# Kernel optimization log

Measured on AMD Instinct MI355X. Metric: run time of the kernel, lower is better.

Reference implementation:

```python
import jax, jax.numpy as jnp
import numpy as np

# dims
B_, L_, DIN, H, DOUT, NL = 2, 1024, 512, 768, 512, 4
ED, N, K = H, 16, 4            # expand_factor=1 -> d_inner=H; d_state=16; d_conv=4
DTR = (H + 15) // 16           # dt_rank = ceil(d_model/16) = 48


def setup_inputs() -> dict:
    key = jax.random.key(0)
    ks = iter(jax.random.split(key, 32))
    def g(shape, s=0.02):
        return jax.random.normal(next(ks), shape, jnp.float32) * s
    inp = dict(
        x=jax.random.normal(next(ks), (B_, L_, DIN), jnp.float32),
        in_proj_w=g((H, DIN)), in_proj_b=jnp.zeros((H,), jnp.float32),
        out_proj_w=g((DOUT, H)), out_proj_b=jnp.zeros((DOUT,), jnp.float32),
        ln1_w=jnp.ones((NL, H), jnp.float32), ln1_b=jnp.zeros((NL, H), jnp.float32),
        ln2_w=jnp.ones((NL, H), jnp.float32), ln2_b=jnp.zeros((NL, H), jnp.float32),
        ffn_w1=g((NL, 4 * H, H)), ffn_b1=jnp.zeros((NL, 4 * H), jnp.float32),
        ffn_w2=g((NL, H, 4 * H)), ffn_b2=jnp.zeros((NL, H), jnp.float32),
        rms_w=jnp.ones((NL, ED), jnp.float32),
        m_in_w=g((NL, 2 * ED, H)),
        conv_w=g((NL, ED, 1, K), 0.2), conv_b=jnp.zeros((NL, ED), jnp.float32),
        xproj_w=g((NL, DTR + 2 * N, ED)),
        dt_w=g((NL, ED, DTR), 0.1), dt_b=g((NL, ED), 0.1),
        A_log=jnp.log(jnp.tile(jnp.arange(1, N + 1, dtype=jnp.float32), (NL, ED, 1))),
        Dp=jnp.ones((NL, ED), jnp.float32),
        m_out_w=g((NL, H, ED)),
    )
    return inp


def _layernorm(x, w, b):
    m = x.mean(-1, keepdims=True)
    v = ((x - m) ** 2).mean(-1, keepdims=True)
    return (x - m) / jnp.sqrt(v + 1e-5) * w + b


def _rmsnorm(x, w):
    return x * jax.lax.rsqrt((x * x).mean(-1, keepdims=True) + 1e-5) * w


def _selective_scan(dA, dBx):
    # h_t = dA_t * h_{t-1} + dBx_t, done as a parallel associative scan over L
    def comb(c1, c2):
        a1, b1 = c1
        a2, b2 = c2
        return a1 * a2, a2 * b1 + b2
    _, h = jax.lax.associative_scan(comb, (dA, dBx), axis=1)
    return h  # (B, L, ED, N)


def _mamba(x, rw, iw, cw, cb, xw, dw, db, Alog, Dp, ow):
    # mambapy ResidualBlock: x + MambaBlock(RMSNorm(x))
    xn = _rmsnorm(x, rw)
    xz = xn @ iw.T                             # (B, L, 2*ED)
    xi, z = jnp.split(xz, 2, axis=-1)
    # causal depthwise conv1d (padding = K-1 left)
    xc = jax.lax.conv_general_dilated(
        xi.transpose(0, 2, 1), cw, (1,), [(K - 1, 0)],
        feature_group_count=ED, dimension_numbers=('NCH', 'OIH', 'NCH'))
    xi = jax.nn.silu(xc.transpose(0, 2, 1) + cb)
    dbc = xi @ xw.T                            # (B, L, DTR + 2N)
    d = dbc[..., :DTR]
    Bm = dbc[..., DTR:DTR + N]
    Cm = dbc[..., DTR + N:]
    delta = jax.nn.softplus(d @ dw.T + db)     # (B, L, ED)
    A = -jnp.exp(Alog)                         # (ED, N)
    dA = jnp.exp(delta[..., None] * A)         # (B, L, ED, N)
    dBx = (delta * xi)[..., None] * Bm[:, :, None, :]
    h = _selective_scan(dA, dBx)
    y = jnp.einsum('blen,bln->ble', h, Cm) + Dp * xi
    y = y * jax.nn.silu(z)
    return x + y @ ow.T


def reference(x, in_proj_w, in_proj_b, out_proj_w, out_proj_b,
              ln1_w, ln1_b, ln2_w, ln2_b,
              ffn_w1, ffn_b1, ffn_w2, ffn_b2,
              rms_w, m_in_w, conv_w, conv_b, xproj_w,
              dt_w, dt_b, A_log, Dp, m_out_w):
    h = x @ in_proj_w.T + in_proj_b
    for i in range(NL):
        h = h + _mamba(_layernorm(h, ln1_w[i], ln1_b[i]),
                       rms_w[i], m_in_w[i], conv_w[i], conv_b[i], xproj_w[i],
                       dt_w[i], dt_b[i], A_log[i], Dp[i], m_out_w[i])
        hn = _layernorm(h, ln2_w[i], ln2_b[i])
        h = h + jax.nn.relu(hn @ ffn_w1[i].T + ffn_b1[i]) @ ffn_w2[i].T + ffn_b2[i]
    return h @ out_proj_w.T + out_proj_b
```

## Files before the change

### kernel.cpp

```cpp
#include <hip/hip_runtime.h>
#include <stdint.h>

typedef unsigned short u16;
typedef __attribute__((ext_vector_type(8))) short short8;
typedef __attribute__((ext_vector_type(4))) float f32x4;

static __device__ __forceinline__ u16 f2bf(float f){
  unsigned int x = __float_as_uint(f);
  unsigned int r = (x + 0x7FFFu + ((x >> 16) & 1u)) >> 16;
  return (u16)r;
}
static __device__ __forceinline__ float bf2f(u16 u){
  return __uint_as_float(((unsigned int)u) << 16);
}

__global__ __launch_bounds__(256) void prep_cvt(
    const float* __restrict__ s0, const float* __restrict__ s1,
    const float* __restrict__ s2, const float* __restrict__ s3,
    const float* __restrict__ s4, const float* __restrict__ s5,
    const float* __restrict__ s6,
    u16* __restrict__ d0, u16* __restrict__ d1, u16* __restrict__ d2,
    u16* __restrict__ d3, u16* __restrict__ d4, u16* __restrict__ d5,
    u16* __restrict__ d6){
  size_t i = ((size_t)blockIdx.x * 256 + threadIdx.x) * 8;
  const float* src; u16* dst; size_t base;
  if      (i <  1048576){ src = s0; dst = d0; base = 0; }
  else if (i <  1441792){ src = s1; dst = d1; base = 1048576; }
  else if (i <  1835008){ src = s2; dst = d2; base = 1441792; }
  else if (i <  6553600){ src = s3; dst = d3; base = 1835008; }
  else if (i <  8912896){ src = s4; dst = d4; base = 6553600; }
  else if (i < 18350080){ src = s5; dst = d5; base = 8912896; }
  else                  { src = s6; dst = d6; base = 18350080; }
  size_t o = i - base;
  #pragma unroll
  for (int p = 0; p < 2; p++){
    float4 v = *reinterpret_cast<const float4*>(src + o + p * 4);
    union { u16 u[4]; unsigned long long ll; } t;
    t.u[0] = f2bf(v.x); t.u[1] = f2bf(v.y); t.u[2] = f2bf(v.z); t.u[3] = f2bf(v.w);
    *reinterpret_cast<unsigned long long*>(dst + o + p * 4) = t.ll;
  }
}

__global__ __launch_bounds__(256) void build_dbc(const float* __restrict__ dt_w,
                                                 const float* __restrict__ xproj_w,
                                                 u16* __restrict__ out){
  const int total = 4 * 896 * 768;
  for (int idx = blockIdx.x * 256 + threadIdx.x; idx < total; idx += gridDim.x * 256){
    int l = idx / (896 * 768);
    int rem = idx - l * 896 * 768;
    int row = rem / 768;
    int k = rem - row * 768;
    float v = 0.f;
    if (row < 768){
      const float* dtr = dt_w + ((size_t)l * 768 + row) * 48;
      const float* xp  = xproj_w + (size_t)l * 80 * 768 + k;
      #pragma unroll 8
      for (int j = 0; j < 48; j++) v += dtr[j] * xp[(size_t)j * 768];
    } else if (row < 800){
      v = xproj_w[(size_t)l * 80 * 768 + (size_t)(48 + row - 768) * 768 + k];
    }
    out[idx] = f2bf(v);
  }
}

__global__ __launch_bounds__(256) void ln_rms_kernel(const float* __restrict__ in,
                                                     const float* __restrict__ w,
                                                     const float* __restrict__ b,
                                                     const float* __restrict__ rw,
                                                     float* __restrict__ xln,
                                                     u16* __restrict__ outB){
  int row = blockIdx.x;
  const float* x = in + (size_t)row * 768;
  int t = threadIdx.x;
  float v0 = x[t], v1 = x[t + 256], v2 = x[t + 512];
  float s = v0 + v1 + v2;
  float s2 = v0 * v0 + v1 * v1 + v2 * v2;
  #pragma unroll
  for (int off = 1; off < 64; off <<= 1){ s += __shfl_xor(s, off); s2 += __shfl_xor(s2, off); }
  __shared__ float red[8];
  int wid = t >> 6, lane = t & 63;
  if (lane == 0){ red[wid] = s; red[4 + wid] = s2; }
  __syncthreads();
  s = red[0] + red[1] + red[2] + red[3];
  s2 = red[4] + red[5] + red[6] + red[7];
  float mean = s * (1.f / 768.f);
  float var = s2 * (1.f / 768.f) - mean * mean;
  float rstd = rsqrtf(var + 1e-5f);
  float o0 = (v0 - mean) * rstd * w[t] + b[t];
  float o1 = (v1 - mean) * rstd * w[t + 256] + b[t + 256];
  float o2 = (v2 - mean) * rstd * w[t + 512] + b[t + 512];
  xln[(size_t)row * 768 + t]       = o0;
  xln[(size_t)row * 768 + t + 256] = o1;
  xln[(size_t)row * 768 + t + 512] = o2;
  float q = o0 * o0 + o1 * o1 + o2 * o2;
  #pragma unroll
  for (int off = 1; off < 64; off <<= 1){ q += __shfl_xor(q, off); }
  __syncthreads();
  if (lane == 0) red[wid] = q;
  __syncthreads();
  q = red[0] + red[1] + red[2] + red[3];
  float rs = rsqrtf(q * (1.f / 768.f) + 1e-5f);
  outB[(size_t)row * 768 + t]       = f2bf(o0 * rs * rw[t]);
  outB[(size_t)row * 768 + t + 256] = f2bf(o1 * rs * rw[t + 256]);
  outB[(size_t)row * 768 + t + 512] = f2bf(o2 * rs * rw[t + 512]);
}

__global__ __launch_bounds__(256) void ln_kernel(const float* __restrict__ in,
                                                 const float* __restrict__ w,
                                                 const float* __restrict__ b,
                                                 u16* __restrict__ outB){
  int row = blockIdx.x;
  const float* x = in + (size_t)row * 768;
  int t = threadIdx.x;
  float v0 = x[t], v1 = x[t + 256], v2 = x[t + 512];
  float s = v0 + v1 + v2;
  float s2 = v0 * v0 + v1 * v1 + v2 * v2;
  #pragma unroll
  for (int off = 1; off < 64; off <<= 1){ s += __shfl_xor(s, off); s2 += __shfl_xor(s2, off); }
  __shared__ float red[8];
  int wid = t >> 6, lane = t & 63;
  if (lane == 0){ red[wid] = s; red[4 + wid] = s2; }
  __syncthreads();
  s = red[0] + red[1] + red[2] + red[3];
  s2 = red[4] + red[5] + red[6] + red[7];
  float mean = s * (1.f / 768.f);
  float var = s2 * (1.f / 768.f) - mean * mean;
  float rstd = rsqrtf(var + 1e-5f);
  #pragma unroll
  for (int j = 0; j < 3; j++){
    int e = t + j * 256;
    float v = (j == 0) ? v0 : (j == 1) ? v1 : v2;
    outB[(size_t)row * 768 + e] = f2bf((v - mean) * rstd * w[e] + b[e]);
  }
}

__global__ __launch_bounds__(256) void conv_silu(const u16* __restrict__ xzb,
                                                 const float* __restrict__ cw,
                                                 const float* __restrict__ cb,
                                                 u16* __restrict__ xi,
                                                 u16* __restrict__ zs){
  int row = blockIdx.x;
  int b = row >> 10, l = row & 1023;
  for (int e = threadIdx.x; e < 768; e += 256){
    const float* w = cw + (size_t)e * 4;
    float acc = cb[e];
    #pragma unroll
    for (int k = 0; k < 4; k++){
      int ls = l - 3 + k;
      if (ls >= 0) acc += w[k] * bf2f(xzb[((size_t)((b << 10) + ls)) * 1536 + e]);
    }
    float sv = acc / (1.f + __expf(-acc));
    xi[(size_t)row * 768 + e] = f2bf(sv);
    float z = bf2f(xzb[(size_t)row * 1536 + 768 + e]);
    zs[(size_t)row * 768 + e] = f2bf(z / (1.f + __expf(-z)));
  }
}

__global__ __launch_bounds__(256) void scan_pass1(const float* __restrict__ delta,
                                                  const u16* __restrict__ xi,
                                                  const float* __restrict__ bc,
                                                  const float* __restrict__ A_log,
                                                  float2* __restrict__ ab){
  int bid = blockIdx.x;
  int eg = bid % 3; int c = (bid / 3) & 31; int b = bid / 96;
  int e = eg * 256 + threadIdx.x;
  float A[16], a[16], s[16];
  const float* al = A_log + (size_t)e * 16;
  #pragma unroll
  for (int n = 0; n < 16; n++){ A[n] = -__expf(al[n]); a[n] = 1.f; s[n] = 0.f; }
  for (int ll = 0; ll < 32; ll++){
    int row = b * 1024 + c * 32 + ll;
    float dlt = delta[(size_t)row * 768 + e];
    float xiv = bf2f(xi[(size_t)row * 768 + e]);
    float du = dlt * xiv;
    const float* bm = bc + (size_t)row * 32;
    #pragma unroll
    for (int n = 0; n < 16; n++){
      float dA = __expf(dlt * A[n]);
      s[n] = dA * s[n] + du * bm[n];
      a[n] *= dA;
    }
  }
  size_t base = (((size_t)(b * 32 + c) * 768) + e) * 16;
  #pragma unroll
  for (int n = 0; n < 16; n++){ ab[base + n] = make_float2(a[n], s[n]); }
}

__global__ __launch_bounds__(128) void scan_pass2(const float2* __restrict__ ab,
                                                  float* __restrict__ h0){
  int idx = blockIdx.x * 128 + threadIdx.x;
  int b = idx / 12288;
  int en = idx - b * 12288;
  float h = 0.f;
  for (int c = 0; c < 32; c++){
    size_t i = ((size_t)(b * 32 + c) * 12288) + en;
    h0[i] = h;
    float2 v = ab[i];
    h = v.x * h + v.y;
  }
}

__global__ __launch_bounds__(256) void scan_pass3(const float* __restrict__ delta,
                                                  const u16* __restrict__ xi,
                                                  const float* __restrict__ bc,
                                                  const float* __restrict__ A_log,
                                                  const float* __restrict__ h0,
                                                  const float* __restrict__ Dp,
                                                  const u16* __restrict__ zs,
                                                  u16* __restrict__ y){
  int bid = blockIdx.x;
  int eg = bid % 3; int c = (bid / 3) & 31; int b = bid / 96;
  int e = eg * 256 + threadIdx.x;
  float A[16], s[16];
  const float* al = A_log + (size_t)e * 16;
  #pragma unroll
  for (int n = 0; n < 16; n++) A[n] = -__expf(al[n]);
  size_t base = (((size_t)(b * 32 + c) * 768) + e) * 16;
  #pragma unroll
  for (int n = 0; n < 16; n++) s[n] = h0[base + n];
  float dp = Dp[e];
  for (int ll = 0; ll < 32; ll++){
    int row = b * 1024 + c * 32 + ll;
    float dlt = delta[(size_t)row * 768 + e];
    float xiv = bf2f(xi[(size_t)row * 768 + e]);
    float du = dlt * xiv;
    const float* bm = bc + (size_t)row * 32;
    const float* cm = bm + 16;
    float acc = 0.f;
    #pragma unroll
    for (int n = 0; n < 16; n++){
      float dA = __expf(dlt * A[n]);
      s[n] = dA * s[n] + du * bm[n];
      acc += s[n] * cm[n];
    }
    float yv = acc + dp * xiv;
    yv *= bf2f(zs[(size_t)row * 768 + e]);
    y[(size_t)row * 768 + e] = f2bf(yv);
  }
}

template<int MODE>
__global__ __launch_bounds__(256, 3) void gemm64(
    const u16* __restrict__ A, const u16* __restrict__ Bw, int N, int Kd,
    float* __restrict__ outF, u16* __restrict__ outB,
    const float* __restrict__ bias, const float* __restrict__ r1,
    const float* __restrict__ r2,
    float* __restrict__ dl, float* __restrict__ bco, const float* __restrict__ dtb){
  __shared__ u16 sm[3][2 * 64 * 64];
  const int tid = threadIdx.x;
  const int wid = tid >> 6, lane = tid & 63;
  const int lhi = lane >> 4, llo = lane & 15;
  const int wm = (wid >> 1) * 32, wn = (wid & 1) * 32;
  int orig = (int)(blockIdx.y * gridDim.x + blockIdx.x);
  int xcd = orig & 7;
  int w = orig >> 3;
  int mt = xcd * 4 + (w & 3);
  int nt = w >> 2;
  const int m0 = mt * 64, n0 = nt * 64;
  const int nk = Kd >> 6;
  f32x4 acc[2][2] = {};

  auto stage = [&](int buf, int kt){
    const u16* Ab = A + (size_t)m0 * Kd + kt * 64;
    const u16* Bb = Bw + (size_t)n0 * Kd + kt * 64;
    u16* basep = &sm[buf][0];
    #pragma unroll
    for (int j = 0; j < 2; j++){
      int sl = j * 256 + tid;
      int row = sl >> 3;
      int ch = (sl & 7) ^ (row & 7);
      __builtin_amdgcn_global_load_lds(
          (const __attribute__((address_space(1))) void*)(Ab + (size_t)row * Kd + ch * 8),
          (__attribute__((address_space(3))) void*)(basep + sl * 8), 16, 0, 0);
    }
    #pragma unroll
    for (int j = 0; j < 2; j++){
      int sl = j * 256 + tid;
      int row = sl >> 3;
      int ch = (sl & 7) ^ (row & 7);
      __builtin_amdgcn_global_load_lds(
          (const __attribute__((address_space(1))) void*)(Bb + (size_t)row * Kd + ch * 8),
          (__attribute__((address_space(3))) void*)(basep + 64 * 64 + sl * 8), 16, 0, 0);
    }
  };

  stage(0, 0);
  stage(1, 1);
  for (int kt = 0; kt < nk; ++kt){
    if (kt + 1 < nk) asm volatile("s_waitcnt vmcnt(4)" ::: "memory");
    else             asm volatile("s_waitcnt vmcnt(0)" ::: "memory");
    __builtin_amdgcn_s_barrier();
    __builtin_amdgcn_sched_barrier(0);
    if (kt + 2 < nk) stage((kt + 2) % 3, kt + 2);
    const u16* Asb = &sm[kt % 3][0];
    const u16* Bsb = &sm[kt % 3][64 * 64];
    short8 af[2][2], bfr[2][2];
    #pragma unroll
    for (int mi = 0; mi < 2; mi++){
      int row = wm + mi * 16 + llo;
      const u16* rp = Asb + row * 64;
      #pragma unroll
      for (int s2 = 0; s2 < 2; s2++){
        int ch = (s2 * 4 + lhi) ^ (row & 7);
        af[mi][s2] = *(const short8*)(rp + ch * 8);
      }
    }
    #pragma unroll
    for (int ni = 0; ni < 2; ni++){
      int row = wn + ni * 16 + llo;
      const u16* rp = Bsb + row * 64;
      #pragma unroll
      for (int s2 = 0; s2 < 2; s2++){
        int ch = (s2 * 4 + lhi) ^ (row & 7);
        bfr[ni][s2] = *(const short8*)(rp + ch * 8);
      }
    }
    __builtin_amdgcn_s_setprio(1);
    #pragma unroll
    for (int s2 = 0; s2 < 2; s2++)
      #pragma unroll
      for (int mi = 0; mi < 2; mi++)
        #pragma unroll
        for (int ni = 0; ni < 2; ni++)
          acc[mi][ni] = __builtin_amdgcn_mfma_f32_16x16x32_bf16(
              af[mi][s2], bfr[ni][s2], acc[mi][ni], 0, 0, 0);
    __builtin_amdgcn_s_setprio(0);
  }
  #pragma unroll
  for (int mi = 0; mi < 2; mi++){
    #pragma unroll
    for (int ni = 0; ni < 2; ni++){
      int r0 = m0 + wm + mi * 16 + lhi * 4;
      int c = n0 + wn + ni * 16 + llo;
      #pragma unroll
      for (int r = 0; r < 4; r++){
        int rr = r0 + r;
        float v = acc[mi][ni][r];
        if (MODE == 0){
          size_t idx = (size_t)rr * N + c;
          if (bias) v += bias[c];
          if (r1) v += r1[idx];
          if (r2) v += r2[idx];
          outF[idx] = v;
          if (outB) outB[idx] = f2bf(v);
        } else if (MODE == 1){
          size_t idx = (size_t)rr * N + c;
          v += bias[c];
          outB[idx] = f2bf(v > 0.f ? v : 0.f);
        } else if (MODE == 3){
          outB[(size_t)rr * N + c] = f2bf(v);
        } else {
          if (c < 768){
            float tv = v + dtb[c];
            dl[(size_t)rr * 768 + c] = (tv > 20.f) ? tv : log1pf(__expf(tv));
          } else if (c < 800){
            bco[(size_t)rr * 32 + (c - 768)] = v;
          }
        }
      }
    }
  }
}

extern "C" void kernel_launch(void* const* d_in, const int* in_sizes, int n_in,
                              void* d_out, int out_size, void* d_ws, size_t ws_size,
                              hipStream_t stream){
  (void)in_sizes; (void)n_in; (void)out_size; (void)ws_size;
  const float* x_f       = (const float*)d_in[0];
  const float* in_proj_w = (const float*)d_in[1];
  const float* in_proj_b = (const float*)d_in[2];
  const float* out_proj_w= (const float*)d_in[3];
  const float* out_proj_b= (const float*)d_in[4];
  const float* ln1_w     = (const float*)d_in[5];
  const float* ln1_b     = (const float*)d_in[6];
  const float* ln2_w     = (const float*)d_in[7];
  const float* ln2_b     = (const float*)d_in[8];
  const float* ffn_w1    = (const float*)d_in[9];
  const float* ffn_b1    = (const float*)d_in[10];
  const float* ffn_w2    = (const float*)d_in[11];
  const float* ffn_b2    = (const float*)d_in[12];
  const float* rms_w     = (const float*)d_in[13];
  const float* m_in_w    = (const float*)d_in[14];
  const float* conv_w    = (const float*)d_in[15];
  const float* conv_b    = (const float*)d_in[16];
  const float* xproj_w   = (const float*)d_in[17];
  const float* dt_w      = (const float*)d_in[18];
  const float* dt_b      = (const float*)d_in[19];
  const float* A_log     = (const float*)d_in[20];
  const float* Dp        = (const float*)d_in[21];
  const float* m_out_w   = (const float*)d_in[22];

  char* ws = (char*)d_ws;
  size_t off = 0;
  auto alloc = [&](size_t bytes) -> char* {
    char* p = ws + off;
    off += (bytes + 255) & ~(size_t)255;
    return p;
  };
  u16* wb_inp  = (u16*)alloc((size_t)768 * 512 * 2);
  u16* wb_outp = (u16*)alloc((size_t)512 * 768 * 2);
  u16* wb_min  = (u16*)alloc((size_t)4 * 1536 * 768 * 2);
  u16* wb_mout = (u16*)alloc((size_t)4 * 768 * 768 * 2);
  u16* wb_f1   = (u16*)alloc((size_t)4 * 3072 * 768 * 2);
  u16* wb_f2   = (u16*)alloc((size_t)4 * 768 * 3072 * 2);
  u16* wb_dbc  = (u16*)alloc((size_t)4 * 896 * 768 * 2);
  u16* xbf     = (u16*)alloc((size_t)2048 * 512 * 2);
  float* hA    = (float*)alloc((size_t)2048 * 768 * 4);
  float* hB    = (float*)alloc((size_t)2048 * 768 * 4);
  float* xln   = (float*)alloc((size_t)2048 * 768 * 4);
  u16* xnbf    = (u16*)alloc((size_t)2048 * 768 * 2);
  u16* xzb     = (u16*)alloc((size_t)2048 * 1536 * 2);
  u16* xibf    = (u16*)alloc((size_t)2048 * 768 * 2);
  u16* zsbf    = (u16*)alloc((size_t)2048 * 768 * 2);
  float* dltb  = (float*)alloc((size_t)2048 * 768 * 4);
  float* bcb   = (float*)alloc((size_t)2048 * 32 * 4);
  float2* ab   = (float2*)alloc((size_t)2 * 32 * 768 * 16 * 8);
  float* h0    = (float*)alloc((size_t)2 * 32 * 768 * 16 * 4);
  u16* ybf     = (u16*)alloc((size_t)2048 * 768 * 2);
  u16* tbf     = (u16*)alloc((size_t)2048 * 768 * 2);
  u16* f1bf    = (u16*)alloc((size_t)2048 * 3072 * 2);
  u16* hfbf    = (u16*)alloc((size_t)2048 * 768 * 2);

  prep_cvt<<<13568, 256, 0, stream>>>(x_f, in_proj_w, out_proj_w, m_in_w,
                                      m_out_w, ffn_w1, ffn_w2,
                                      xbf, wb_inp, wb_outp, wb_min,
                                      wb_mout, wb_f1, wb_f2);
  build_dbc<<<2048, 256, 0, stream>>>(dt_w, xproj_w, wb_dbc);

  auto gemm = [&](int mode, const u16* Ain, const u16* Bww, int N, int K,
                  float* oF, u16* oB, const float* bias, const float* rr1,
                  const float* rr2, float* dl, float* bco, const float* dtb){
    dim3 g(32, N / 64), blk(256);
    if (mode == 0)
      gemm64<0><<<g, blk, 0, stream>>>(Ain, Bww, N, K, oF, oB, bias, rr1, rr2, dl, bco, dtb);
    else if (mode == 1)
      gemm64<1><<<g, blk, 0, stream>>>(Ain, Bww, N, K, oF, oB, bias, rr1, rr2, dl, bco, dtb);
    else if (mode == 2)
      gemm64<2><<<g, blk, 0, stream>>>(Ain, Bww, N, K, oF, oB, bias, rr1, rr2, dl, bco, dtb);
    else
      gemm64<3><<<g, blk, 0, stream>>>(Ain, Bww, N, K, oF, oB, bias, rr1, rr2, dl, bco, dtb);
  };

  gemm(0, xbf, wb_inp, 768, 512, hA, nullptr, in_proj_b, nullptr, nullptr,
       nullptr, nullptr, nullptr);

  for (int i = 0; i < 4; i++){
    ln_rms_kernel<<<2048, 256, 0, stream>>>(hA, ln1_w + i * 768, ln1_b + i * 768,
                                            rms_w + i * 768, xln, xnbf);
    gemm(3, xnbf, wb_min + (size_t)i * 1536 * 768, 1536, 768, nullptr, xzb,
         nullptr, nullptr, nullptr, nullptr, nullptr, nullptr);
    conv_silu<<<2048, 256, 0, stream>>>(xzb, conv_w + (size_t)i * 768 * 4,
                                        conv_b + i * 768, xibf, zsbf);
    gemm(2, xibf, wb_dbc + (size_t)i * 896 * 768, 896, 768, nullptr, nullptr,
         nullptr, nullptr, nullptr, dltb, bcb, dt_b + i * 768);
    scan_pass1<<<192, 256, 0, stream>>>(dltb, xibf, bcb,
                                        A_log + (size_t)i * 768 * 16, ab);
    scan_pass2<<<192, 128, 0, stream>>>(ab, h0);
    scan_pass3<<<192, 256, 0, stream>>>(dltb, xibf, bcb,
                                        A_log + (size_t)i * 768 * 16, h0,
                                        Dp + i * 768, zsbf, ybf);
    gemm(0, ybf, wb_mout + (size_t)i * 768 * 768, 768, 768, hB, nullptr,
         nullptr, hA, xln, nullptr, nullptr, nullptr);
    ln_kernel<<<2048, 256, 0, stream>>>(hB, ln2_w + i * 768, ln2_b + i * 768, tbf);
    gemm(1, tbf, wb_f1 + (size_t)i * 3072 * 768, 3072, 768, nullptr, f1bf,
         ffn_b1 + i * 3072, nullptr, nullptr, nullptr, nullptr, nullptr);
    gemm(0, f1bf, wb_f2 + (size_t)i * 768 * 3072, 768, 3072, hA,
         (i == 3) ? hfbf : nullptr, ffn_b2 + i * 768, hB, nullptr,
         nullptr, nullptr, nullptr);
  }
  gemm(0, hfbf, wb_outp, 512, 768, (float*)d_out, nullptr, out_proj_b,
       nullptr, nullptr, nullptr, nullptr, nullptr);
}
```

Baseline: 680.8 us.

## Split-K the FFN down-projection and fuse partial-sum reduction into next LayerNorm

The FFN second GEMM (K=3072, only 384 tiles) now runs with a 4-way split over K, writing fp32 partial results to a scratch buffer. The partials, bias and residual are summed inside the next layer's LN/RMS kernel, or in a new final reduction kernel before the output projection. This targets low occupancy and the long serial K loop of that GEMM, at the cost of extra fp32 traffic for four partial buffers. Separately, the weight conversion kernel now has each block process a 16K-element chunk with strided float4 accesses instead of 8 elements per thread.

```diff
diff --git a/kernel.cpp b/kernel.cpp
--- a/kernel.cpp
+++ b/kernel.cpp
@@ -22,22 +22,22 @@
     u16* __restrict__ d0, u16* __restrict__ d1, u16* __restrict__ d2,
     u16* __restrict__ d3, u16* __restrict__ d4, u16* __restrict__ d5,
     u16* __restrict__ d6){
-  size_t i = ((size_t)blockIdx.x * 256 + threadIdx.x) * 8;
+  size_t blk = (size_t)blockIdx.x * 16384;
   const float* src; u16* dst; size_t base;
-  if      (i <  1048576){ src = s0; dst = d0; base = 0; }
-  else if (i <  1441792){ src = s1; dst = d1; base = 1048576; }
-  else if (i <  1835008){ src = s2; dst = d2; base = 1441792; }
-  else if (i <  6553600){ src = s3; dst = d3; base = 1835008; }
-  else if (i <  8912896){ src = s4; dst = d4; base = 6553600; }
-  else if (i < 18350080){ src = s5; dst = d5; base = 8912896; }
-  else                  { src = s6; dst = d6; base = 18350080; }
-  size_t o = i - base;
-  #pragma unroll
-  for (int p = 0; p < 2; p++){
-    float4 v = *reinterpret_cast<const float4*>(src + o + p * 4);
+  if      (blk <  1048576){ src = s0; dst = d0; base = 0; }
+  else if (blk <  1441792){ src = s1; dst = d1; base = 1048576; }
+  else if (blk <  1835008){ src = s2; dst = d2; base = 1441792; }
+  else if (blk <  6553600){ src = s3; dst = d3; base = 1835008; }
+  else if (blk <  8912896){ src = s4; dst = d4; base = 6553600; }
+  else if (blk < 18350080){ src = s5; dst = d5; base = 8912896; }
+  else                    { src = s6; dst = d6; base = 18350080; }
+  size_t o = blk - base + (size_t)threadIdx.x * 4;
+  #pragma unroll
+  for (int p = 0; p < 16; p++){
+    float4 v = *reinterpret_cast<const float4*>(src + o + (size_t)p * 1024);
     union { u16 u[4]; unsigned long long ll; } t;
     t.u[0] = f2bf(v.x); t.u[1] = f2bf(v.y); t.u[2] = f2bf(v.z); t.u[3] = f2bf(v.w);
-    *reinterpret_cast<unsigned long long*>(dst + o + p * 4) = t.ll;
+    *reinterpret_cast<unsigned long long*>(dst + o + (size_t)p * 1024) = t.ll;
   }
 }
 
@@ -64,17 +64,34 @@
 }
 
 __global__ __launch_bounds__(256) void ln_rms_kernel(const float* __restrict__ in,
+                                                     const float* __restrict__ parts,
+                                                     const float* __restrict__ hres,
+                                                     const float* __restrict__ fb2,
                                                      const float* __restrict__ w,
                                                      const float* __restrict__ b,
                                                      const float* __restrict__ rw,
                                                      float* __restrict__ xln,
+                                                     float* __restrict__ hout,
                                                      u16* __restrict__ outB){
   int row = blockIdx.x;
-  const float* x = in + (size_t)row * 768;
   int t = threadIdx.x;
-  float v0 = x[t], v1 = x[t + 256], v2 = x[t + 512];
-  float s = v0 + v1 + v2;
-  float s2 = v0 * v0 + v1 * v1 + v2 * v2;
+  const size_t PS = (size_t)2048 * 768;
+  float v[3];
+  #pragma unroll
+  for (int j = 0; j < 3; j++){
+    int e = t + j * 256;
+    size_t idx = (size_t)row * 768 + e;
+    if (parts){
+      float sv = parts[idx] + parts[idx + PS] + parts[idx + 2 * PS] + parts[idx + 3 * PS]
+               + fb2[e] + hres[idx];
+      hout[idx] = sv;
+      v[j] = sv;
+    } else {
+      v[j] = in[idx];
+    }
+  }
+  float s = v[0] + v[1] + v[2];
+  float s2 = v[0] * v[0] + v[1] * v[1] + v[2] * v[2];
   #pragma unroll
   for (int off = 1; off < 64; off <<= 1){ s += __shfl_xor(s, off); s2 += __shfl_xor(s2, off); }
   __shared__ float red[8];
@@ -86,9 +103,9 @@
   float mean = s * (1.f / 768.f);
   float var = s2 * (1.f / 768.f) - mean * mean;
   float rstd = rsqrtf(var + 1e-5f);
-  float o0 = (v0 - mean) * rstd * w[t] + b[t];
-  float o1 = (v1 - mean) * rstd * w[t + 256] + b[t + 256];
-  float o2 = (v2 - mean) * rstd * w[t + 512] + b[t + 512];
+  float o0 = (v[0] - mean) * rstd * w[t] + b[t];
+  float o1 = (v[1] - mean) * rstd * w[t + 256] + b[t + 256];
+  float o2 = (v[2] - mean) * rstd * w[t + 512] + b[t + 512];
   xln[(size_t)row * 768 + t]       = o0;
   xln[(size_t)row * 768 + t + 256] = o1;
   xln[(size_t)row * 768 + t + 512] = o2;
@@ -103,6 +120,18 @@
   outB[(size_t)row * 768 + t]       = f2bf(o0 * rs * rw[t]);
   outB[(size_t)row * 768 + t + 256] = f2bf(o1 * rs * rw[t + 256]);
   outB[(size_t)row * 768 + t + 512] = f2bf(o2 * rs * rw[t + 512]);
+}
+
+__global__ __launch_bounds__(256) void reduce_final(const float* __restrict__ parts,
+                                                    const float* __restrict__ hres,
+                                                    const float* __restrict__ fb2,
+                                                    u16* __restrict__ outB){
+  size_t idx = (size_t)blockIdx.x * 256 + threadIdx.x;
+  const size_t PS = (size_t)2048 * 768;
+  int e = (int)(idx % 768);
+  float sv = parts[idx] + parts[idx + PS] + parts[idx + 2 * PS] + parts[idx + 3 * PS]
+           + fb2[e] + hres[idx];
+  outB[idx] = f2bf(sv);
 }
 
 __global__ __launch_bounds__(256) void ln_kernel(const float* __restrict__ in,
@@ -257,7 +286,10 @@
   int mt = xcd * 4 + (w & 3);
   int nt = w >> 2;
   const int m0 = mt * 64, n0 = nt * 64;
-  const int nk = Kd >> 6;
+  int nk = Kd >> 6;
+  int per = nk / (int)gridDim.z;
+  int k0 = (int)blockIdx.z * per;
+  int kend = k0 + per;
   f32x4 acc[2][2] = {};
 
   auto stage = [&](int buf, int kt){
@@ -284,16 +316,17 @@
     }
   };
 
-  stage(0, 0);
-  stage(1, 1);
-  for (int kt = 0; kt < nk; ++kt){
-    if (kt + 1 < nk) asm volatile("s_waitcnt vmcnt(4)" ::: "memory");
-    else             asm volatile("s_waitcnt vmcnt(0)" ::: "memory");
+  stage(0, k0);
+  stage(1, k0 + 1);
+  for (int kt = k0; kt < kend; ++kt){
+    if (kt + 1 < kend) asm volatile("s_waitcnt vmcnt(4)" ::: "memory");
+    else               asm volatile("s_waitcnt vmcnt(0)" ::: "memory");
     __builtin_amdgcn_s_barrier();
     __builtin_amdgcn_sched_barrier(0);
-    if (kt + 2 < nk) stage((kt + 2) % 3, kt + 2);
-    const u16* Asb = &sm[kt % 3][0];
-    const u16* Bsb = &sm[kt % 3][64 * 64];
+    if (kt + 2 < kend) stage((kt - k0 + 2) % 3, kt + 2);
+    int cb = (kt - k0) % 3;
+    const u16* Asb = &sm[cb][0];
+    const u16* Bsb = &sm[cb][64 * 64];
     short8 af[2][2], bfr[2][2];
     #pragma unroll
     for (int mi = 0; mi < 2; mi++){
@@ -349,6 +382,8 @@
           outB[idx] = f2bf(v > 0.f ? v : 0.f);
         } else if (MODE == 3){
           outB[(size_t)rr * N + c] = f2bf(v);
+        } else if (MODE == 4){
+          dl[((size_t)blockIdx.z * 2048 + rr) * N + c] = v;
         } else {
           if (c < 768){
             float tv = v + dtb[c];
@@ -420,17 +455,18 @@
   u16* tbf     = (u16*)alloc((size_t)2048 * 768 * 2);
   u16* f1bf    = (u16*)alloc((size_t)2048 * 3072 * 2);
   u16* hfbf    = (u16*)alloc((size_t)2048 * 768 * 2);
-
-  prep_cvt<<<13568, 256, 0, stream>>>(x_f, in_proj_w, out_proj_w, m_in_w,
-                                      m_out_w, ffn_w1, ffn_w2,
-                                      xbf, wb_inp, wb_outp, wb_min,
-                                      wb_mout, wb_f1, wb_f2);
+  float* parts = (float*)alloc((size_t)4 * 2048 * 768 * 4);
+
+  prep_cvt<<<1696, 256, 0, stream>>>(x_f, in_proj_w, out_proj_w, m_in_w,
+                                     m_out_w, ffn_w1, ffn_w2,
+                                     xbf, wb_inp, wb_outp, wb_min,
+                                     wb_mout, wb_f1, wb_f2);
   build_dbc<<<2048, 256, 0, stream>>>(dt_w, xproj_w, wb_dbc);
 
   auto gemm = [&](int mode, const u16* Ain, const u16* Bww, int N, int K,
                   float* oF, u16* oB, const float* bias, const float* rr1,
                   const float* rr2, float* dl, float* bco, const float* dtb){
-    dim3 g(32, N / 64), blk(256);
+    dim3 g(32, N / 64, 1), blk(256);
     if (mode == 0)
       gemm64<0><<<g, blk, 0, stream>>>(Ain, Bww, N, K, oF, oB, bias, rr1, rr2, dl, bco, dtb);
     else if (mode == 1)
@@ -445,8 +481,14 @@
        nullptr, nullptr, nullptr);
 
   for (int i = 0; i < 4; i++){
-    ln_rms_kernel<<<2048, 256, 0, stream>>>(hA, ln1_w + i * 768, ln1_b + i * 768,
-                                            rms_w + i * 768, xln, xnbf);
+    if (i == 0)
+      ln_rms_kernel<<<2048, 256, 0, stream>>>(hA, nullptr, nullptr, nullptr,
+                                              ln1_w, ln1_b, rms_w, xln, hA, xnbf);
+    else
+      ln_rms_kernel<<<2048, 256, 0, stream>>>(nullptr, parts, hB,
+                                              ffn_b2 + (i - 1) * 768,
+                                              ln1_w + i * 768, ln1_b + i * 768,
+                                              rms_w + i * 768, xln, hA, xnbf);
     gemm(3, xnbf, wb_min + (size_t)i * 1536 * 768, 1536, 768, nullptr, xzb,
          nullptr, nullptr, nullptr, nullptr, nullptr, nullptr);
     conv_silu<<<2048, 256, 0, stream>>>(xzb, conv_w + (size_t)i * 768 * 4,
@@ -464,10 +506,14 @@
     ln_kernel<<<2048, 256, 0, stream>>>(hB, ln2_w + i * 768, ln2_b + i * 768, tbf);
     gemm(1, tbf, wb_f1 + (size_t)i * 3072 * 768, 3072, 768, nullptr, f1bf,
          ffn_b1 + i * 3072, nullptr, nullptr, nullptr, nullptr, nullptr);
-    gemm(0, f1bf, wb_f2 + (size_t)i * 768 * 3072, 768, 3072, hA,
-         (i == 3) ? hfbf : nullptr, ffn_b2 + i * 768, hB, nullptr,
-         nullptr, nullptr, nullptr);
-  }
+    {
+      dim3 g(32, 12, 4), blk(256);
+      gemm64<4><<<g, blk, 0, stream>>>(f1bf, wb_f2 + (size_t)i * 768 * 3072, 768, 3072,
+                                       nullptr, nullptr, nullptr, nullptr, nullptr,
+                                       parts, nullptr, nullptr);
+    }
+  }
+  reduce_final<<<6144, 256, 0, stream>>>(parts, hB, ffn_b2 + 3 * 768, hfbf);
   gemm(0, hfbf, wb_outp, 512, 768, (float*)d_out, nullptr, out_proj_b,
        nullptr, nullptr, nullptr, nullptr, nullptr);
 }
```

Result: no change. 684.3 us (+0.5%).
